# Kernel optimization log

Hardware: AMD Instinct MI355X
Metric: run time of the kernel (lower is better)

The kernel has to match this reference:

```python
import jax, jax.numpy as jnp
import numpy as np

N = 100_000   # num nodes
E = 3_200_000 # num directed edges (before self-loops)
NEG_SLOPE = 0.2


def setup_inputs() -> dict:
    key = jax.random.key(0)
    ks = jax.random.split(key, 12)
    x = jax.random.normal(ks[0], (N, 2), jnp.float32)
    edge_index = jax.random.randint(ks[1], (2, E), 0, N, dtype=jnp.int32)
    # GATConv(2, 16): lin weight [2,16] (no bias), att_src/att_dst [16], out bias [16]
    W1 = jax.random.normal(ks[2], (2, 16), jnp.float32) * (1.0 / np.sqrt(2.0))
    a_src1 = jax.random.normal(ks[3], (16,), jnp.float32) * 0.25
    a_dst1 = jax.random.normal(ks[4], (16,), jnp.float32) * 0.25
    b1 = jnp.zeros((16,), jnp.float32)
    # GATConv(16, 64)
    W2 = jax.random.normal(ks[5], (16, 64), jnp.float32) * (1.0 / np.sqrt(16.0))
    a_src2 = jax.random.normal(ks[6], (64,), jnp.float32) * 0.125
    a_dst2 = jax.random.normal(ks[7], (64,), jnp.float32) * 0.125
    b2 = jnp.zeros((64,), jnp.float32)
    return {"x": x, "edge_index": edge_index,
            "W1": W1, "a_src1": a_src1, "a_dst1": a_dst1, "b1": b1,
            "W2": W2, "a_src2": a_src2, "a_dst2": a_dst2, "b2": b2}


def _gat_layer(x, src, dst, W, a_src, a_dst, b):
    # x: [N, Fin]; src/dst: [E'] (self-loops included). Single head, PyG GATConv math.
    h = x @ W                                        # [N, Fout]
    alpha_s = h @ a_src                              # [N]
    alpha_d = h @ a_dst                              # [N]
    e = jax.nn.leaky_relu(alpha_s[src] + alpha_d[dst], NEG_SLOPE)  # [E']
    # segment softmax over incoming edges of each dst node
    m = jax.ops.segment_max(e, dst, num_segments=N)
    m = jnp.where(jnp.isfinite(m), m, 0.0)           # nodes always have a self-loop, but be safe
    p = jnp.exp(e - m[dst])
    s = jax.ops.segment_sum(p, dst, num_segments=N)
    alpha = p / s[dst]                               # [E']
    out = jax.ops.segment_sum(alpha[:, None] * h[src], dst, num_segments=N)  # [N, Fout]
    return out + b


def reference(x, edge_index, W1, a_src1, a_dst1, b1, W2, a_src2, a_dst2, b2):
    # PyG GATConv adds self-loops by default
    loops = jnp.arange(N, dtype=edge_index.dtype)
    src = jnp.concatenate([edge_index[0], loops])
    dst = jnp.concatenate([edge_index[1], loops])
    h = jax.nn.relu(_gat_layer(x, src, dst, W1, a_src1, a_dst1, b1))
    h = jax.nn.relu(_gat_layer(h, src, dst, W2, a_src2, a_dst2, b2))
    return h
```

## Files before the change

kernel.cpp:

```cpp
#include <hip/hip_runtime.h>

#define NNODES 100000
#define NEDGES 3200000
#define ETOT   (NEDGES + NNODES)
#define NEG_SLOPE 0.2f

#define NPB 64
#define NBUCK ((NNODES + NPB - 1) / NPB)
#define NCHUNK 256
#define CHUNK_E ((ETOT + NCHUNK - 1) / NCHUNK)
#define M2 (NBUCK * NCHUNK)
#define NSB2 ((M2 + 511) / 512)

__device__ __forceinline__ unsigned short f2bf(float f) {
    unsigned u = __float_as_uint(f);
    u += 0x7FFFu + ((u >> 16) & 1u);
    return (unsigned short)(u >> 16);
}
__device__ __forceinline__ float bf2f(unsigned short h) {
    return __uint_as_float(((unsigned)h) << 16);
}

__device__ __forceinline__ void edge_sd(int e, const int* __restrict__ ei, int& s, int& d) {
    if (e < NEDGES) { s = ei[e]; d = ei[NEDGES + e]; }
    else            { s = e - NEDGES; d = s; }
}

__device__ __forceinline__ float lrelu(float v) {
    return v > 0.0f ? v : NEG_SLOPE * v;
}

__device__ __forceinline__ float bcast_lane(float v, int lane_imm) {
    return __int_as_float(__builtin_amdgcn_readlane(__float_as_int(v), lane_imm));
}

template<int CTRL>
__device__ __forceinline__ float dpp_add(float v) {
    return v + __int_as_float(__builtin_amdgcn_mov_dpp(__float_as_int(v), CTRL, 0xF, 0xF, true));
}
__device__ __forceinline__ float swz16_add(float v) {
    return v + __int_as_float(__builtin_amdgcn_ds_swizzle(__float_as_int(v), 0x401F));
}
__device__ __forceinline__ float row16_sum(float v) {
    v = dpp_add<0x121>(v);
    v = dpp_add<0x122>(v);
    v = dpp_add<0x124>(v);
    v = dpp_add<0x128>(v);
    return v;
}


__global__ void chunk_hist(const int* __restrict__ ei, int* __restrict__ H) {
    __shared__ int h[NBUCK];
    int c = blockIdx.x;
    for (int i = threadIdx.x; i < NBUCK; i += blockDim.x) h[i] = 0;
    __syncthreads();
    int lo = c * CHUNK_E, hi = lo + CHUNK_E; if (hi > ETOT) hi = ETOT;
    for (int e = lo + threadIdx.x; e < hi; e += blockDim.x) {
        int d = (e < NEDGES) ? ei[NEDGES + e] : (e - NEDGES);
        atomicAdd(&h[d >> 6], 1);
    }
    __syncthreads();
    for (int i = threadIdx.x; i < NBUCK; i += blockDim.x) H[c * NBUCK + i] = h[i];
}

__global__ void cscan_local(const int* __restrict__ H, int* __restrict__ off,
                            int* __restrict__ bsum2) {
    __shared__ int arr[512];
    int blk = blockIdx.x, t = threadIdx.x;
    int i = blk * 512 + t;
    int v = (i < M2) ? H[(i & (NCHUNK - 1)) * NBUCK + (i >> 8)] : 0;
    arr[t] = v;
    __syncthreads();
    for (int o = 1; o < 512; o <<= 1) {
        int u = (t >= o) ? arr[t - o] : 0;
        __syncthreads();
        arr[t] += u;
        __syncthreads();
    }
    if (i < M2) off[i] = arr[t] - v;
    if (t == 511) bsum2[blk] = arr[t];
}

__global__ void cscan_bsum(const int* __restrict__ bsum2, int* __restrict__ boff2) {
    __shared__ int arr[1024];
    int t = threadIdx.x;
    int v = (t < NSB2) ? bsum2[t] : 0;
    arr[t] = v;
    __syncthreads();
    for (int o = 1; o < 1024; o <<= 1) {
        int u = (t >= o) ? arr[t - o] : 0;
        __syncthreads();
        arr[t] += u;
        __syncthreads();
    }
    if (t < NSB2) boff2[t] = arr[t] - v;
}

__global__ void cscan_add(int* __restrict__ off, const int* __restrict__ boff2) {
    int i = blockIdx.x * 512 + threadIdx.x;
    if (i < M2) off[i] += boff2[blockIdx.x];
}

__global__ __launch_bounds__(1024)
void chunk_scatter(const int* __restrict__ ei, const int* __restrict__ off,
                   const int* __restrict__ H, int* __restrict__ pairs) {
    __shared__ int plds[CHUNK_E];
    __shared__ unsigned short blds[CHUNK_E];
    __shared__ int sc[2048];
    __shared__ int lcur[NBUCK];
    __shared__ int gbase[NBUCK];
    int c = blockIdx.x, t = threadIdx.x;
    for (int b = t; b < 2048; b += 1024) sc[b] = (b < NBUCK) ? H[c * NBUCK + b] : 0;
    __syncthreads();
    for (int o = 1; o < 2048; o <<= 1) {
        int i1 = t + 1024;
        int v0 = (t >= o) ? sc[t - o] : 0;
        int v1 = (i1 >= o) ? sc[i1 - o] : 0;
        __syncthreads();
        sc[t] += v0; sc[i1] += v1;
        __syncthreads();
    }
    for (int b = t; b < NBUCK; b += 1024) {
        int excl = (b == 0) ? 0 : sc[b - 1];
        lcur[b]  = excl;
        gbase[b] = off[b * NCHUNK + c] - excl;
    }
    __syncthreads();
    int lo = c * CHUNK_E, hi = lo + CHUNK_E; if (hi > ETOT) hi = ETOT;
    int n = hi - lo;
    for (int e = lo + t; e < hi; e += 1024) {
        int s, d; edge_sd(e, ei, s, d);
        int b = d >> 6;
        int slot = atomicAdd(&lcur[b], 1);
        plds[slot] = ((d & 63) << 17) | s;
        blds[slot] = (unsigned short)b;
    }
    __syncthreads();
    for (int i = t; i < n; i += 1024)
        pairs[gbase[blds[i]] + i] = plds[i];
}

__global__ void fine_sort2(const int* __restrict__ off, const int* __restrict__ pairs,
                           int* __restrict__ row_start, int* __restrict__ csr_src) {
    __shared__ int arr[NPB];
    __shared__ int cur[NPB];
    int b = blockIdx.x;
    int t = threadIdx.x;
    int base = off[b * NCHUNK];
    int bend = (b == NBUCK - 1) ? ETOT : off[(b + 1) * NCHUNK];
    if (t < NPB) arr[t] = 0;
    __syncthreads();
    for (int i = base + t; i < bend; i += blockDim.x)
        atomicAdd(&arr[pairs[i] >> 17], 1);
    __syncthreads();
    int v = (t < NPB) ? arr[t] : 0;
    __syncthreads();
    for (int o = 1; o < NPB; o <<= 1) {
        int u = (t < NPB && t >= o) ? arr[t - o] : 0;
        __syncthreads();
        if (t < NPB) arr[t] += u;
        __syncthreads();
    }
    if (t < NPB) {
        int node = b * NPB + t;
        int start = base + arr[t] - v;
        cur[t] = start;
        if (node < NNODES) row_start[node] = start;
    }
    if (b == NBUCK - 1 && t == 0) row_start[NNODES] = ETOT;
    __syncthreads();
    for (int i = base + t; i < bend; i += blockDim.x) {
        int p = pairs[i];
        int slot = atomicAdd(&cur[p >> 17], 1);
        csr_src[slot] = p & 0x1FFFF;
    }
}

__global__ void prep(const float* __restrict__ W1, const float* __restrict__ as1,
                     const float* __restrict__ ad1, const float* __restrict__ W2,
                     const float* __restrict__ as2, const float* __restrict__ ad2,
                     float* __restrict__ cvec) {
    int t = threadIdx.x;
    if (t < 2) {
        float s = 0.f, d = 0.f;
        for (int f = 0; f < 16; ++f) { s += W1[t * 16 + f] * as1[f]; d += W1[t * 16 + f] * ad1[f]; }
        cvec[t] = s; cvec[2 + t] = d;
    }
    if (t < 16) {
        float s = 0.f, d = 0.f;
        for (int f = 0; f < 64; ++f) { s += W2[t * 64 + f] * as2[f]; d += W2[t * 64 + f] * ad2[f]; }
        cvec[4 + t] = s; cvec[20 + t] = d;
    }
}

__global__ void alpha1(const float* __restrict__ x, const float* __restrict__ cvec,
                       float* __restrict__ as_, float* __restrict__ ad_) {
    int n = blockIdx.x * blockDim.x + threadIdx.x;
    if (n >= NNODES) return;
    float2 xv = ((const float2*)x)[n];
    as_[n] = xv.x * cvec[0] + xv.y * cvec[1];
    ad_[n] = xv.x * cvec[2] + xv.y * cvec[3];
}

__global__ void agg_l1(const int* __restrict__ row_start, const int* __restrict__ csr_src,
                       const float* __restrict__ as_, const float* __restrict__ ad_,
                       const float* __restrict__ x, const float* __restrict__ W1,
                       const float* __restrict__ b1, const float* __restrict__ cvec,
                       unsigned short* __restrict__ g,
                       float* __restrict__ as2_, float* __restrict__ ad2_) {
    int wave = threadIdx.x >> 6, lane = threadIdx.x & 63;
    int node = blockIdx.x * 4 + wave;
    int base = row_start[node], end = row_start[node + 1];
    float adv = ad_[node];
    float a0 = 0.f, a1 = 0.f, ss = 0.f;
    const float2* x2 = (const float2*)x;
    int last = end - 1;
    int i = base + lane;
    int sj = csr_src[min(i, last)];
    float asv = as_[sj];
    float2 xv = x2[sj];
    while (i < end) {
        int inext = i + 64;
        int sjn = csr_src[min(inext, last)];
        float asn = as_[sjn];
        float2 xn = x2[sjn];
        float w = __expf(lrelu(asv + adv));
        ss += w;
        a0 += w * xv.x;
        a1 += w * xv.y;
        i = inext; sj = sjn; asv = asn; xv = xn;
    }
    a0 = row16_sum(a0); a1 = row16_sum(a1); ss = row16_sum(ss);
    a0 = swz16_add(a0); a1 = swz16_add(a1); ss = swz16_add(ss);
    a0 += __shfl_xor(a0, 32);
    a1 += __shfl_xor(a1, 32);
    ss += __shfl_xor(ss, 32);
    int f = lane & 15;
    float v = (a0 * W1[f] + a1 * W1[16 + f]) / ss + b1[f];
    float vr = v > 0.f ? v : 0.f;
    if (lane < 16) g[node * 16 + lane] = f2bf(vr);
    float s2 = vr * cvec[4 + f];
    float d2 = vr * cvec[20 + f];
    s2 = row16_sum(s2); d2 = row16_sum(d2);
    if (lane == 0) { as2_[node] = s2; ad2_[node] = d2; }
}

__global__ void agg_l2(const int* __restrict__ row_start, const int* __restrict__ csr_src,
                       const float* __restrict__ as_, const float* __restrict__ ad_,
                       const unsigned short* __restrict__ g, const float* __restrict__ W2,
                       const float* __restrict__ b2, float* __restrict__ out) {
    int wave = threadIdx.x >> 6, lane = threadIdx.x & 63;
    int grp = lane >> 2;
    int q   = lane & 3;
    int node = blockIdx.x * 4 + wave;
    int base = row_start[node], end = row_start[node + 1];
    float adv = ad_[node];
    float a0 = 0.f, a1 = 0.f, a2 = 0.f, a3 = 0.f, ss = 0.f;
    int last = end - 1;
    int i = base + grp;
    int sj = csr_src[min(i, last)];
    float asv = as_[sj];
    ushort4 hv = ((const ushort4*)(g + sj * 16))[q];
    while (i < end) {
        int inext = i + 16;
        int sjn = csr_src[min(inext, last)];
        float asn = as_[sjn];
        ushort4 hn = ((const ushort4*)(g + sjn * 16))[q];
        float w = __expf(lrelu(asv + adv));
        ss += w;
        a0 += w * bf2f(hv.x);
        a1 += w * bf2f(hv.y);
        a2 += w * bf2f(hv.z);
        a3 += w * bf2f(hv.w);
        i = inext; sj = sjn; asv = asn; hv = hn;
    }
    a0 = dpp_add<0x124>(a0); a1 = dpp_add<0x124>(a1);
    a2 = dpp_add<0x124>(a2); a3 = dpp_add<0x124>(a3); ss = dpp_add<0x124>(ss);
    a0 = dpp_add<0x128>(a0); a1 = dpp_add<0x128>(a1);
    a2 = dpp_add<0x128>(a2); a3 = dpp_add<0x128>(a3); ss = dpp_add<0x128>(ss);
    a0 = swz16_add(a0); a1 = swz16_add(a1);
    a2 = swz16_add(a2); a3 = swz16_add(a3); ss = swz16_add(ss);
    a0 += __shfl_xor(a0, 32);
    a1 += __shfl_xor(a1, 32);
    a2 += __shfl_xor(a2, 32);
    a3 += __shfl_xor(a3, 32);
    ss += __shfl_xor(ss, 32);
    float o = 0.f;
#pragma unroll
    for (int k = 0; k < 16; ++k) {
        float aqsel = (k & 3) == 0 ? a0 : ((k & 3) == 1 ? a1 : ((k & 3) == 2 ? a2 : a3));
        float rk = bcast_lane(aqsel, k >> 2);
        o += rk * W2[k * 64 + lane];
    }
    o = o / ss + b2[lane];
    out[(size_t)node * 64 + lane] = o > 0.f ? o : 0.f;
}

extern "C" void kernel_launch(void* const* d_in, const int* in_sizes, int n_in,
                              void* d_out, int out_size, void* d_ws, size_t ws_size,
                              hipStream_t stream) {
    const float* x     = (const float*)d_in[0];
    const int*   ei    = (const int*)  d_in[1];
    const float* W1    = (const float*)d_in[2];
    const float* as1w  = (const float*)d_in[3];
    const float* ad1w  = (const float*)d_in[4];
    const float* b1    = (const float*)d_in[5];
    const float* W2    = (const float*)d_in[6];
    const float* as2w  = (const float*)d_in[7];
    const float* ad2w  = (const float*)d_in[8];
    const float* b2    = (const float*)d_in[9];
    float* out = (float*)d_out;

    int* row_start = (int*)d_ws;
    int* csr_src   = row_start + (NNODES + 4);
    float* gslot   = (float*)(csr_src + ETOT);
    unsigned short* gbuf = (unsigned short*)gslot;
    float* asb     = gslot + (size_t)NNODES * 16;
    float* adb     = asb + NNODES;
    float* as2b    = adb + NNODES;
    float* ad2b    = as2b + NNODES;
    float* cvec    = ad2b + NNODES;
    int* pairs     = (int*)(cvec + 64);
    int* H         = pairs + ETOT;
    int* off       = H + M2;
    int* bsum2     = off + M2;
    int* boff2     = bsum2 + 1024;

    const int B = 256;
    const int NB = (NNODES + B - 1) / B;

    chunk_hist<<<NCHUNK, 1024, 0, stream>>>(ei, H);
    cscan_local<<<NSB2, 512, 0, stream>>>(H, off, bsum2);
    cscan_bsum<<<1, 1024, 0, stream>>>(bsum2, boff2);
    cscan_add<<<NSB2, 512, 0, stream>>>(off, boff2);
    chunk_scatter<<<NCHUNK, 1024, 0, stream>>>(ei, off, H, pairs);
    fine_sort2<<<NBUCK, B, 0, stream>>>(off, pairs, row_start, csr_src);

    prep<<<1, 64, 0, stream>>>(W1, as1w, ad1w, W2, as2w, ad2w, cvec);

    alpha1<<<NB, B, 0, stream>>>(x, cvec, asb, adb);
    agg_l1<<<NNODES / 4, B, 0, stream>>>(row_start, csr_src, asb, adb, x, W1, b1,
                                         cvec, gbuf, as2b, ad2b);

    agg_l2<<<NNODES / 4, B, 0, stream>>>(row_start, csr_src, as2b, ad2b, gbuf, W2, b2, out);
}
```

Baseline: 240.6 us.

## Process one edge per lane in layer-2 aggregation with full 16-feature accumulators

```diff
diff --git a/kernel.cpp b/kernel.cpp
--- a/kernel.cpp
+++ b/kernel.cpp
@@ -30,10 +30,6 @@
     return v > 0.0f ? v : NEG_SLOPE * v;
 }
 
-__device__ __forceinline__ float bcast_lane(float v, int lane_imm) {
-    return __int_as_float(__builtin_amdgcn_readlane(__float_as_int(v), lane_imm));
-}
-
 template<int CTRL>
 __device__ __forceinline__ float dpp_add(float v) {
     return v + __int_as_float(__builtin_amdgcn_mov_dpp(__float_as_int(v), CTRL, 0xF, 0xF, true));
@@ -46,6 +42,12 @@
     v = dpp_add<0x122>(v);
     v = dpp_add<0x124>(v);
     v = dpp_add<0x128>(v);
+    return v;
+}
+__device__ __forceinline__ float wave64_sum(float v) {
+    v = row16_sum(v);
+    v = swz16_add(v);
+    v += __shfl_xor(v, 32);
     return v;
 }
 
@@ -231,11 +233,7 @@
         a1 += w * xv.y;
         i = inext; sj = sjn; asv = asn; xv = xn;
     }
-    a0 = row16_sum(a0); a1 = row16_sum(a1); ss = row16_sum(ss);
-    a0 = swz16_add(a0); a1 = swz16_add(a1); ss = swz16_add(ss);
-    a0 += __shfl_xor(a0, 32);
-    a1 += __shfl_xor(a1, 32);
-    ss += __shfl_xor(ss, 32);
+    a0 = wave64_sum(a0); a1 = wave64_sum(a1); ss = wave64_sum(ss);
     int f = lane & 15;
     float v = (a0 * W1[f] + a1 * W1[16 + f]) / ss + b1[f];
     float vr = v > 0.f ? v : 0.f;
@@ -251,48 +249,33 @@
                        const unsigned short* __restrict__ g, const float* __restrict__ W2,
                        const float* __restrict__ b2, float* __restrict__ out) {
     int wave = threadIdx.x >> 6, lane = threadIdx.x & 63;
-    int grp = lane >> 2;
-    int q   = lane & 3;
     int node = blockIdx.x * 4 + wave;
     int base = row_start[node], end = row_start[node + 1];
     float adv = ad_[node];
-    float a0 = 0.f, a1 = 0.f, a2 = 0.f, a3 = 0.f, ss = 0.f;
-    int last = end - 1;
-    int i = base + grp;
-    int sj = csr_src[min(i, last)];
-    float asv = as_[sj];
-    ushort4 hv = ((const ushort4*)(g + sj * 16))[q];
-    while (i < end) {
-        int inext = i + 16;
-        int sjn = csr_src[min(inext, last)];
-        float asn = as_[sjn];
-        ushort4 hn = ((const ushort4*)(g + sjn * 16))[q];
-        float w = __expf(lrelu(asv + adv));
+    float acc[16];
+#pragma unroll
+    for (int k = 0; k < 16; ++k) acc[k] = 0.f;
+    float ss = 0.f;
+    for (int i = base + lane; i < end; i += 64) {
+        int sj = csr_src[i];
+        float w = __expf(lrelu(as_[sj] + adv));
         ss += w;
-        a0 += w * bf2f(hv.x);
-        a1 += w * bf2f(hv.y);
-        a2 += w * bf2f(hv.z);
-        a3 += w * bf2f(hv.w);
-        i = inext; sj = sjn; asv = asn; hv = hn;
-    }
-    a0 = dpp_add<0x124>(a0); a1 = dpp_add<0x124>(a1);
-    a2 = dpp_add<0x124>(a2); a3 = dpp_add<0x124>(a3); ss = dpp_add<0x124>(ss);
-    a0 = dpp_add<0x128>(a0); a1 = dpp_add<0x128>(a1);
-    a2 = dpp_add<0x128>(a2); a3 = dpp_add<0x128>(a3); ss = dpp_add<0x128>(ss);
-    a0 = swz16_add(a0); a1 = swz16_add(a1);
-    a2 = swz16_add(a2); a3 = swz16_add(a3); ss = swz16_add(ss);
-    a0 += __shfl_xor(a0, 32);
-    a1 += __shfl_xor(a1, 32);
-    a2 += __shfl_xor(a2, 32);
-    a3 += __shfl_xor(a3, 32);
-    ss += __shfl_xor(ss, 32);
+        const uint4* gp = (const uint4*)(g + sj * 16);
+        uint4 u0 = gp[0], u1 = gp[1];
+        unsigned uu[8] = {u0.x, u0.y, u0.z, u0.w, u1.x, u1.y, u1.z, u1.w};
+#pragma unroll
+        for (int j = 0; j < 8; ++j) {
+            acc[2 * j]     += w * __uint_as_float(uu[j] << 16);
+            acc[2 * j + 1] += w * __uint_as_float(uu[j] & 0xFFFF0000u);
+        }
+    }
+#pragma unroll
+    for (int k = 0; k < 16; ++k) acc[k] = wave64_sum(acc[k]);
+    ss = wave64_sum(ss);
     float o = 0.f;
 #pragma unroll
-    for (int k = 0; k < 16; ++k) {
-        float aqsel = (k & 3) == 0 ? a0 : ((k & 3) == 1 ? a1 : ((k & 3) == 2 ? a2 : a3));
-        float rk = bcast_lane(aqsel, k >> 2);
-        o += rk * W2[k * 64 + lane];
-    }
+    for (int k = 0; k < 16; ++k)
+        o += acc[k] * W2[k * 64 + lane];
     o = o / ss + b2[lane];
     out[(size_t)node * 64 + lane] = o > 0.f ? o : 0.f;
 }
```

Result: no change. 242.7 us (+0.9%).
